# Optimization experiments

Hardware: AMD Instinct MI355X
Metric: run time of the kernel (lower is better)

## Reference

```python
import jax, jax.numpy as jnp
import numpy as np

N, C, E, T, H, D = 50000, 128, 320000, 8, 64, 4
EPS = 1e-5


def setup_inputs() -> dict:
    key = jax.random.key(0)
    ks = jax.random.split(key, 10)
    x = jax.random.normal(ks[0], (N, C), dtype=jnp.float32)
    edge_index = jax.random.randint(ks[1], (2, E), 0, N, dtype=jnp.int64)
    edge_types = jax.random.randint(ks[2], (E,), 0, T, dtype=jnp.int64)
    # per-type MLP params: LayerNorm(2C) -> Linear(2C,H) -> ReLU -> Linear(H, D*D)
    s1 = 1.0 / np.sqrt(2 * C)
    s2 = 1.0 / np.sqrt(H)
    gamma = jnp.ones((T, 2 * C), dtype=jnp.float32)
    beta = jnp.zeros((T, 2 * C), dtype=jnp.float32)
    W1 = jax.random.uniform(ks[3], (T, 2 * C, H), jnp.float32, -s1, s1)
    b1 = jax.random.uniform(ks[4], (T, H), jnp.float32, -s1, s1)
    W2 = jax.random.uniform(ks[5], (T, H, D * D), jnp.float32, -s2, s2)
    b2 = jax.random.uniform(ks[6], (T, D * D), jnp.float32, -s2, s2)
    return {"x": x, "edge_index": edge_index, "edge_types": edge_types,
            "gamma": gamma, "beta": beta, "W1": W1, "b1": b1, "W2": W2, "b2": b2}


def reference(x, edge_index, edge_types, gamma, beta, W1, b1, W2, b2):
    row, col = edge_index[0], edge_index[1]
    h_cat = jnp.concatenate([x[row], x[col]], axis=-1)  # [E, 2C]
    # shared (non-affine) layernorm stats; per-type affine applied in the loop
    mu = jnp.mean(h_cat, axis=-1, keepdims=True)
    var = jnp.mean(jnp.square(h_cat - mu), axis=-1, keepdims=True)
    x_hat = (h_cat - mu) * jax.lax.rsqrt(var + EPS)  # [E, 2C]
    out = jnp.zeros((E, D * D), dtype=h_cat.dtype)
    for t in range(T):  # fixed, small structural loop over edge types
        h = x_hat * gamma[t] + beta[t]
        h1 = jax.nn.relu(h @ W1[t] + b1[t])  # [E, H]
        o = h1 @ W2[t] + b2[t]               # [E, D*D]
        out = jnp.where((edge_types == t)[:, None], o, out)
    h_sheaf = out.reshape(-1, D, D)
    attn = jax.nn.softmax(h_sheaf, axis=-1)
    sheaf_maps = jnp.eye(D, dtype=h_sheaf.dtype)[None] - attn
    return sheaf_maps
```

## Files before the change

### kernel.cpp

```cpp
#include <hip/hip_runtime.h>
#include <math.h>

#define CC 128
#define TWO_C 256
#define NT 8
#define HH 64
#define DD 16

typedef short bf16x8 __attribute__((ext_vector_type(8)));
typedef float f32x4 __attribute__((ext_vector_type(4)));

static __device__ __forceinline__ unsigned short f2bf_rne(float f) {
    union { float f; unsigned int u; } v; v.f = f;
    unsigned int r = (v.u + 0x7fffu + ((v.u >> 16) & 1u)) >> 16;
    return (unsigned short)r;
}
static __device__ __forceinline__ unsigned int pkbf(float a, float b) {
    unsigned int ua = __float_as_uint(a) + 0x8000u;
    unsigned int ub = __float_as_uint(b) + 0x8000u;
    return (ua >> 16) | (ub & 0xffff0000u);
}
static __device__ __forceinline__ void glds16(const void* g, void* l) {
    __builtin_amdgcn_global_load_lds(
        (const __attribute__((address_space(1))) void*)g,
        (__attribute__((address_space(3))) void*)l, 16, 0, 0);
}

__global__ __launch_bounds__(256) void pack_kernel(
    const float* __restrict__ W1, const float* __restrict__ W2,
    const float* __restrict__ gamma, const float* __restrict__ beta,
    const float* __restrict__ b1, const float* __restrict__ x,
    unsigned short* __restrict__ W1p, unsigned short* __restrict__ W2p,
    float* __restrict__ s1g, float* __restrict__ c1g,
    unsigned short* __restrict__ xb, float2* __restrict__ SQ, int Nnodes)
{
    const int tid = blockIdx.x * 256 + threadIdx.x;

    if (tid < 16384) {
        int l = tid & 63, kt = (tid >> 6) & 7, nt = (tid >> 9) & 3, t = tid >> 11;
        int n = nt * 16 + (l & 15);
        int k0 = kt * 32 + (l >> 4) * 8;
        #pragma unroll
        for (int j = 0; j < 8; ++j) {
            int k = k0 + j;
            float v = gamma[t * TWO_C + k] * W1[(size_t)t * TWO_C * HH + (size_t)k * HH + n];
            W1p[tid * 8 + j] = f2bf_rne(v);
        }
    } else if (tid < 17408) {
        int s = tid - 16384;
        int l = s & 63, kt = (s >> 6) & 1, t = s >> 7;
        int n = l & 15;
        int k0 = kt * 32 + (l >> 4) * 8;
        #pragma unroll
        for (int j = 0; j < 8; ++j)
            W2p[s * 8 + j] = f2bf_rne(W2[(size_t)t * HH * DD + (size_t)(k0 + j) * DD + n]);
    } else if (tid < 17920) {
        int s = tid - 17408;
        int t = s >> 6, n = s & 63;
        float sa = 0.f, ca = 0.f;
        for (int k = 0; k < TWO_C; ++k) {
            float wv = W1[(size_t)t * TWO_C * HH + (size_t)k * HH + n];
            sa = fmaf(gamma[t * TWO_C + k], wv, sa);
            ca = fmaf(beta[t * TWO_C + k], wv, ca);
        }
        s1g[s] = sa;
        c1g[s] = ca + b1[s];
    } else {
        int idx = tid - 17920;
        int v = idx >> 4;
        if (v < Nnodes) {
            int ll = idx & 15;
            int base = idx * 8;
            float4 p = *(const float4*)(x + base);
            float4 q = *(const float4*)(x + base + 4);
            uint4 u;
            u.x = pkbf(p.x, p.y); u.y = pkbf(p.z, p.w);
            u.z = pkbf(q.x, q.y); u.w = pkbf(q.z, q.w);
            *(uint4*)(xb + base) = u;
            float s  = p.x + p.y + p.z + p.w + q.x + q.y + q.z + q.w;
            float sq = p.x*p.x + p.y*p.y + p.z*p.z + p.w*p.w
                     + q.x*q.x + q.y*q.y + q.z*q.z + q.w*q.w;
            #pragma unroll
            for (int off = 1; off < 16; off <<= 1) {
                s  += __shfl_xor(s, off);
                sq += __shfl_xor(sq, off);
            }
            if (ll == 0) SQ[v] = make_float2(s, sq);
        }
    }
}

__global__ __launch_bounds__(256) void hist_kernel(const int* __restrict__ et,
                                                   int* __restrict__ counts, int E)
{
    __shared__ int lh[NT];
    if (threadIdx.x < NT) lh[threadIdx.x] = 0;
    __syncthreads();
    int i0 = (blockIdx.x * 256 + threadIdx.x) * 4;
    if (i0 + 3 < E) {
        int4 tv = *(const int4*)(et + i0);
        atomicAdd(&lh[tv.x], 1); atomicAdd(&lh[tv.y], 1);
        atomicAdd(&lh[tv.z], 1); atomicAdd(&lh[tv.w], 1);
    } else {
        #pragma unroll
        for (int j = 0; j < 4; ++j)
            if (i0 + j < E) atomicAdd(&lh[et[i0 + j]], 1);
    }
    __syncthreads();
    if (threadIdx.x < NT && lh[threadIdx.x]) atomicAdd(&counts[threadIdx.x], lh[threadIdx.x]);
}

__global__ void scan_kernel(const int* __restrict__ counts, int* __restrict__ po,
                            int* __restrict__ cursor)
{
    if (threadIdx.x == 0 && blockIdx.x == 0) {
        int acc = 0;
        for (int t = 0; t < NT; ++t) {
            po[t] = acc;
            cursor[t] = acc;
            acc += ((counts[t] + 63) >> 6) << 6;
        }
        po[NT] = acc;
    }
}

__global__ __launch_bounds__(256) void scatter_kernel(const int* __restrict__ et,
                                                      const int* __restrict__ ei,
                                                      int* __restrict__ cursor,
                                                      int* __restrict__ sorted,
                                                      int* __restrict__ srow,
                                                      int* __restrict__ scol,
                                                      int* __restrict__ inv,
                                                      int E, int write_inv)
{
    __shared__ int lh[NT], lbase[NT];
    if (threadIdx.x < NT) lh[threadIdx.x] = 0;
    __syncthreads();
    int i0 = (blockIdx.x * 256 + threadIdx.x) * 4;
    int tl[4], rk[4];
    #pragma unroll
    for (int j = 0; j < 4; ++j) {
        int i = i0 + j;
        if (i < E) { tl[j] = et[i]; rk[j] = atomicAdd(&lh[tl[j]], 1); }
    }
    __syncthreads();
    if (threadIdx.x < NT)
        lbase[threadIdx.x] = lh[threadIdx.x] ? atomicAdd(&cursor[threadIdx.x], lh[threadIdx.x]) : 0;
    __syncthreads();
    #pragma unroll
    for (int j = 0; j < 4; ++j) {
        int i = i0 + j;
        if (i < E) {
            int slot = lbase[tl[j]] + rk[j];
            sorted[slot] = i;
            srow[slot] = ei[i];
            scol[slot] = ei[E + i];
            if (write_inv) inv[i] = slot;
        }
    }
}

#define XHAT_OFF 0
#define H1_OFF   0
#define STATS_OFF 16384
#define SID_OFF   16896
#define RB_OFF    17152
#define CB_OFF    17408
#define LDS_BYTES 17664

template <int TMP>
__global__ __launch_bounds__(256, 8) void sheaf_main_full(
    const unsigned short* __restrict__ xb, const float* __restrict__ b2,
    const unsigned short* __restrict__ W1p, const unsigned short* __restrict__ W2p,
    const float* __restrict__ s1g, const float* __restrict__ c1g,
    const float2* __restrict__ SQ,
    const int* __restrict__ po, const int* __restrict__ counts,
    const int* __restrict__ sorted, const int* __restrict__ srow,
    const int* __restrict__ scol,
    float* __restrict__ dst)
{
    __shared__ __align__(16) unsigned char lds[LDS_BYTES];
    const int base = blockIdx.x * 64;
    if (base >= po[NT]) return;
    int t = 0;
    while (base >= po[t + 1]) ++t;
    const int lim = po[t] + counts[t];
    if (base >= lim) return;

    const int tid = threadIdx.x;
    const int w = tid >> 6, lane = tid & 63;
    const int lg = lane >> 4, ll = lane & 15;

    int* sid  = (int*)(lds + SID_OFF);
    int* rbuf = (int*)(lds + RB_OFF);
    int* cbuf = (int*)(lds + CB_OFF);
    float2* stats = (float2*)(lds + STATS_OFF);

    if (tid < 64) {
        int slot = base + tid;
        int src = slot < lim ? slot : po[t];
        rbuf[tid] = srow[src];
        cbuf[tid] = scol[src];
        if (!TMP) sid[tid] = sorted[src];
    }
    __syncthreads();

    #pragma unroll
    for (int i = 0; i < 4; ++i) {
        const int el = w * 16 + i * 4 + lg;
        const unsigned short* src = xb + (size_t)rbuf[el] * CC + ((ll ^ (el & 7)) * 8);
        glds16(src, lds + XHAT_OFF + (w * 16 + i * 4) * 256);
    }
    if (tid < 64) {
        float2 a = SQ[rbuf[tid]];
        float2 b = SQ[cbuf[tid]];
        float mu  = (a.x + b.x) * (1.0f / TWO_C);
        float var = (a.y + b.y) * (1.0f / TWO_C) - mu * mu;
        stats[tid] = make_float2(mu, rsqrtf(var + 1e-5f));
    }
    __syncthreads();

    f32x4 acc[4];
    #pragma unroll
    for (int mt = 0; mt < 4; ++mt) acc[mt] = (f32x4){0.f, 0.f, 0.f, 0.f};
    const bf16x8* Bp = (const bf16x8*)W1p + (size_t)((t * 4 + w) * 8) * 64 + lane;
    #pragma unroll
    for (int kt = 0; kt < 4; ++kt) {
        bf16x8 bfrag = Bp[kt * 64];
        #pragma unroll
        for (int mt = 0; mt < 4; ++mt) {
            int row = mt * 16 + ll;
            bf16x8 afrag = *(const bf16x8*)(lds + XHAT_OFF + row * 256 +
                                            ((kt * 64 + lg * 16) ^ ((row & 7) << 4)));
            acc[mt] = __builtin_amdgcn_mfma_f32_16x16x32_bf16(afrag, bfrag, acc[mt], 0, 0, 0);
        }
    }
    __syncthreads();

    #pragma unroll
    for (int i = 0; i < 4; ++i) {
        const int el = w * 16 + i * 4 + lg;
        const unsigned short* src = xb + (size_t)cbuf[el] * CC + ((ll ^ (el & 7)) * 8);
        glds16(src, lds + XHAT_OFF + (w * 16 + i * 4) * 256);
    }
    __syncthreads();

    #pragma unroll
    for (int kt = 0; kt < 4; ++kt) {
        bf16x8 bfrag = Bp[(4 + kt) * 64];
        #pragma unroll
        for (int mt = 0; mt < 4; ++mt) {
            int row = mt * 16 + ll;
            bf16x8 afrag = *(const bf16x8*)(lds + XHAT_OFF + row * 256 +
                                            ((kt * 64 + lg * 16) ^ ((row & 7) << 4)));
            acc[mt] = __builtin_amdgcn_mfma_f32_16x16x32_bf16(afrag, bfrag, acc[mt], 0, 0, 0);
        }
    }
    __syncthreads();

    const int n = w * 16 + ll;
    const float s1v = s1g[t * HH + n];
    const float c1v = c1g[t * HH + n];
    #pragma unroll
    for (int mt = 0; mt < 4; ++mt) {
        #pragma unroll
        for (int j = 0; j < 4; ++j) {
            int el = mt * 16 + lg * 4 + j;
            float2 st = stats[el];
            float z = st.y * (acc[mt][j] - st.x * s1v) + c1v;
            z = fmaxf(z, 0.0f);
            *(unsigned short*)(lds + H1_OFF + el * 144 + n * 2) =
                (unsigned short)((__float_as_uint(z) + 0x8000u) >> 16);
        }
    }
    __syncthreads();

    f32x4 acc2 = (f32x4){0.f, 0.f, 0.f, 0.f};
    #pragma unroll
    for (int kt = 0; kt < 2; ++kt) {
        bf16x8 bfrag = ((const bf16x8*)W2p)[(t * 2 + kt) * 64 + lane];
        bf16x8 afrag = *(const bf16x8*)(lds + H1_OFF + (w * 16 + ll) * 144 + kt * 64 + lg * 16);
        acc2 = __builtin_amdgcn_mfma_f32_16x16x32_bf16(afrag, bfrag, acc2, 0, 0, 0);
    }

    const float b2v = b2[t * DD + ll];
    const float diag = ((ll >> 2) == (ll & 3)) ? 1.0f : 0.0f;
    #pragma unroll
    for (int j = 0; j < 4; ++j) {
        float o = acc2[j] + b2v;
        float m = fmaxf(o, __shfl_xor(o, 1));
        m = fmaxf(m, __shfl_xor(m, 2));
        float p = __expf(o - m);
        float su = p + __shfl_xor(p, 1);
        su += __shfl_xor(su, 2);
        float res = diag - p / su;
        int el = w * 16 + lg * 4 + j;
        if (TMP) dst[(size_t)(base + el) * DD + ll] = res;
        else     dst[(size_t)sid[el] * DD + ll] = res;
    }
}

__global__ __launch_bounds__(256, 8) void sheaf_main_fb(
    const float* __restrict__ x, const float* __restrict__ b2,
    const unsigned short* __restrict__ W1p, const unsigned short* __restrict__ W2p,
    const float* __restrict__ s1g, const float* __restrict__ c1g,
    const int* __restrict__ po, const int* __restrict__ counts,
    const int* __restrict__ sorted, const int* __restrict__ srow,
    const int* __restrict__ scol,
    float* __restrict__ out)
{
    __shared__ __align__(16) unsigned char lds[LDS_BYTES];
    const int base = blockIdx.x * 64;
    if (base >= po[NT]) return;
    int t = 0;
    while (base >= po[t + 1]) ++t;
    const int lim = po[t] + counts[t];
    if (base >= lim) return;

    const int tid = threadIdx.x;
    const int w = tid >> 6, lane = tid & 63;
    const int lg = lane >> 4, ll = lane & 15;
    int* sid  = (int*)(lds + SID_OFF);
    int* rbuf = (int*)(lds + RB_OFF);
    int* cbuf = (int*)(lds + CB_OFF);

    if (tid < 64) {
        int slot = base + tid;
        int src = slot < lim ? slot : po[t];
        rbuf[tid] = srow[src]; cbuf[tid] = scol[src]; sid[tid] = sorted[src];
    }
    __syncthreads();

    float s[4] = {0,0,0,0}, sq[4] = {0,0,0,0};
    #pragma unroll
    for (int i = 0; i < 4; ++i) {
        const int el = w * 16 + i * 4 + lg;
        const float4* px = (const float4*)(x + (size_t)rbuf[el] * CC + ll * 8);
        float4 p = px[0], q = px[1];
        s[i] += p.x+p.y+p.z+p.w+q.x+q.y+q.z+q.w;
        sq[i] = fmaf(p.x,p.x,sq[i]); sq[i] = fmaf(p.y,p.y,sq[i]);
        sq[i] = fmaf(p.z,p.z,sq[i]); sq[i] = fmaf(p.w,p.w,sq[i]);
        sq[i] = fmaf(q.x,q.x,sq[i]); sq[i] = fmaf(q.y,q.y,sq[i]);
        sq[i] = fmaf(q.z,q.z,sq[i]); sq[i] = fmaf(q.w,q.w,sq[i]);
        uint4 u;
        u.x = pkbf(p.x,p.y); u.y = pkbf(p.z,p.w); u.z = pkbf(q.x,q.y); u.w = pkbf(q.z,q.w);
        *(uint4*)(lds + XHAT_OFF + el * 256 + ((ll * 16) ^ ((el & 7) << 4))) = u;
    }
    __syncthreads();

    f32x4 acc[4];
    #pragma unroll
    for (int mt = 0; mt < 4; ++mt) acc[mt] = (f32x4){0.f,0.f,0.f,0.f};
    const bf16x8* Bp = (const bf16x8*)W1p + (size_t)((t * 4 + w) * 8) * 64 + lane;
    #pragma unroll
    for (int kt = 0; kt < 4; ++kt) {
        bf16x8 bfrag = Bp[kt * 64];
        #pragma unroll
        for (int mt = 0; mt < 4; ++mt) {
            int row = mt * 16 + ll;
            bf16x8 afrag = *(const bf16x8*)(lds + XHAT_OFF + row * 256 +
                                            ((kt * 64 + lg * 16) ^ ((row & 7) << 4)));
            acc[mt] = __builtin_amdgcn_mfma_f32_16x16x32_bf16(afrag, bfrag, acc[mt], 0, 0, 0);
        }
    }
    __syncthreads();

    #pragma unroll
    for (int i = 0; i < 4; ++i) {
        const int el = w * 16 + i * 4 + lg;
        const float4* px = (const float4*)(x + (size_t)cbuf[el] * CC + ll * 8);
        float4 p = px[0], q = px[1];
        s[i] += p.x+p.y+p.z+p.w+q.x+q.y+q.z+q.w;
        sq[i] = fmaf(p.x,p.x,sq[i]); sq[i] = fmaf(p.y,p.y,sq[i]);
        sq[i] = fmaf(p.z,p.z,sq[i]); sq[i] = fmaf(p.w,p.w,sq[i]);
        sq[i] = fmaf(q.x,q.x,sq[i]); sq[i] = fmaf(q.y,q.y,sq[i]);
        sq[i] = fmaf(q.z,q.z,sq[i]); sq[i] = fmaf(q.w,q.w,sq[i]);
        uint4 u;
        u.x = pkbf(p.x,p.y); u.y = pkbf(p.z,p.w); u.z = pkbf(q.x,q.y); u.w = pkbf(q.z,q.w);
        *(uint4*)(lds + XHAT_OFF + el * 256 + ((ll * 16) ^ ((el & 7) << 4))) = u;
    }
    float2* stats = (float2*)(lds + STATS_OFF);
    #pragma unroll
    for (int i = 0; i < 4; ++i) {
        float s_ = s[i], q_ = sq[i];
        #pragma unroll
        for (int off = 1; off < 16; off <<= 1) {
            s_ += __shfl_xor(s_, off); q_ += __shfl_xor(q_, off);
        }
        if (ll == 0) {
            float mu = s_ * (1.0f / TWO_C);
            float var = q_ * (1.0f / TWO_C) - mu * mu;
            stats[w * 16 + i * 4 + lg] = make_float2(mu, rsqrtf(var + 1e-5f));
        }
    }
    __syncthreads();

    #pragma unroll
    for (int kt = 0; kt < 4; ++kt) {
        bf16x8 bfrag = Bp[(4 + kt) * 64];
        #pragma unroll
        for (int mt = 0; mt < 4; ++mt) {
            int row = mt * 16 + ll;
            bf16x8 afrag = *(const bf16x8*)(lds + XHAT_OFF + row * 256 +
                                            ((kt * 64 + lg * 16) ^ ((row & 7) << 4)));
            acc[mt] = __builtin_amdgcn_mfma_f32_16x16x32_bf16(afrag, bfrag, acc[mt], 0, 0, 0);
        }
    }
    __syncthreads();

    const int n = w * 16 + ll;
    const float s1v = s1g[t * HH + n];
    const float c1v = c1g[t * HH + n];
    #pragma unroll
    for (int mt = 0; mt < 4; ++mt) {
        #pragma unroll
        for (int j = 0; j < 4; ++j) {
            int el = mt * 16 + lg * 4 + j;
            float2 st = stats[el];
            float z = st.y * (acc[mt][j] - st.x * s1v) + c1v;
            z = fmaxf(z, 0.0f);
            *(unsigned short*)(lds + H1_OFF + el * 144 + n * 2) =
                (unsigned short)((__float_as_uint(z) + 0x8000u) >> 16);
        }
    }
    __syncthreads();

    f32x4 acc2 = (f32x4){0.f,0.f,0.f,0.f};
    #pragma unroll
    for (int kt = 0; kt < 2; ++kt) {
        bf16x8 bfrag = ((const bf16x8*)W2p)[(t * 2 + kt) * 64 + lane];
        bf16x8 afrag = *(const bf16x8*)(lds + H1_OFF + (w * 16 + ll) * 144 + kt * 64 + lg * 16);
        acc2 = __builtin_amdgcn_mfma_f32_16x16x32_bf16(afrag, bfrag, acc2, 0, 0, 0);
    }
    const float b2v = b2[t * DD + ll];
    const float diag = ((ll >> 2) == (ll & 3)) ? 1.0f : 0.0f;
    #pragma unroll
    for (int j = 0; j < 4; ++j) {
        float o = acc2[j] + b2v;
        float m = fmaxf(o, __shfl_xor(o, 1));
        m = fmaxf(m, __shfl_xor(m, 2));
        float p = __expf(o - m);
        float su = p + __shfl_xor(p, 1);
        su += __shfl_xor(su, 2);
        int el = w * 16 + lg * 4 + j;
        out[(size_t)sid[el] * DD + ll] = diag - p / su;
    }
}

__global__ __launch_bounds__(256) void permute_kernel(const float4* __restrict__ tmp,
                                                      const int* __restrict__ inv,
                                                      float4* __restrict__ out, int E)
{
    int e = blockIdx.x * 256 + threadIdx.x;
    if (e >= E) return;
    int slot = inv[e];
    const float4* s = tmp + (size_t)slot * 4;
    float4 a = s[0], b = s[1], c = s[2], d = s[3];
    float4* o = out + (size_t)e * 4;
    o[0] = a; o[1] = b; o[2] = c; o[3] = d;
}

extern "C" void kernel_launch(void* const* d_in, const int* in_sizes, int n_in,
                              void* d_out, int out_size, void* d_ws, size_t ws_size,
                              hipStream_t stream) {
    const float* x          = (const float*)d_in[0];
    const int*   edge_index = (const int*)  d_in[1];
    const int*   edge_types = (const int*)  d_in[2];
    const float* gamma      = (const float*)d_in[3];
    const float* beta       = (const float*)d_in[4];
    const float* W1         = (const float*)d_in[5];
    const float* b1         = (const float*)d_in[6];
    const float* W2         = (const float*)d_in[7];
    const float* b2         = (const float*)d_in[8];
    float* out = (float*)d_out;

    const int E = in_sizes[2];
    const int xtotal = in_sizes[0];
    const int Nn = xtotal / CC;
    const int cap = ((E + 63) & ~63) + 512;

    int* ws_i   = (int*)d_ws;
    int* counts = ws_i;
    int* cursor = ws_i + 16;
    int* po     = ws_i + 24;
    int* sorted = ws_i + 40;
    int* srow   = sorted + cap;
    int* scol   = srow + cap;

    const size_t pack_bytes = (size_t)NT * 4 * 8 * 64 * 8 * 2
                            + (size_t)NT * 2 * 64 * 8 * 2
                            + (size_t)NT * HH * 4 * 2;
    size_t pk_off = (((size_t)(40 + 3 * (size_t)cap)) * 4 + 255) & ~(size_t)255;
    unsigned short* W1p = (unsigned short*)((char*)d_ws + pk_off);
    unsigned short* W2p = W1p + (size_t)NT * 4 * 8 * 64 * 8;
    float* s1g = (float*)(W2p + (size_t)NT * 2 * 64 * 8);
    float* c1g = s1g + NT * HH;

    size_t sq_off = (pk_off + pack_bytes + 255) & ~(size_t)255;
    float2* SQ = (float2*)((char*)d_ws + sq_off);
    size_t xb_off = (sq_off + (size_t)Nn * 8 + 255) & ~(size_t)255;
    unsigned short* xb = (unsigned short*)((char*)d_ws + xb_off);
    const size_t xb_end = xb_off + (size_t)xtotal * 2;

    const int use_full = (ws_size >= xb_end) ? 1 : 0;

    size_t inv_off = (xb_end + 255) & ~(size_t)255;
    size_t tmp_off = (inv_off + (size_t)cap * 4 + 255) & ~(size_t)255;
    const int use_tmp = (use_full && ws_size >= tmp_off + (size_t)cap * DD * 4) ? 1 : 0;
    int* inv = (int*)((char*)d_ws + inv_off);
    float* tmp = (float*)((char*)d_ws + tmp_off);

    hipMemsetAsync(counts, 0, 32, stream);

    const int pt = use_full ? (17920 + Nn * 16) : 17920;
    hipLaunchKernelGGL(pack_kernel, dim3((pt + 255) / 256), dim3(256), 0, stream,
                       W1, W2, gamma, beta, b1, x, W1p, W2p, s1g, c1g,
                       xb, SQ, use_full ? Nn : 0);

    const int hq = (E + 3) / 4;
    hipLaunchKernelGGL(hist_kernel, dim3((hq + 255) / 256), dim3(256), 0, stream,
                       edge_types, counts, E);
    hipLaunchKernelGGL(scan_kernel, dim3(1), dim3(64), 0, stream, counts, po, cursor);
    hipLaunchKernelGGL(scatter_kernel, dim3((hq + 255) / 256), dim3(256), 0, stream,
                       edge_types, edge_index, cursor, sorted, srow, scol, inv, E, use_tmp);

    const int gmain = cap / 64;
    if (use_full) {
        if (use_tmp) {
            hipLaunchKernelGGL((sheaf_main_full<1>), dim3(gmain), dim3(256), 0, stream,
                               xb, b2, W1p, W2p, s1g, c1g, SQ, po, counts,
                               sorted, srow, scol, tmp);
            hipLaunchKernelGGL(permute_kernel, dim3((E + 255) / 256), dim3(256), 0, stream,
                               (const float4*)tmp, inv, (float4*)out, E);
        } else {
            hipLaunchKernelGGL((sheaf_main_full<0>), dim3(gmain), dim3(256), 0, stream,
                               xb, b2, W1p, W2p, s1g, c1g, SQ, po, counts,
                               sorted, srow, scol, out);
        }
    } else {
        hipLaunchKernelGGL(sheaf_main_fb, dim3(gmain), dim3(256), 0, stream,
                           x, b2, W1p, W2p, s1g, c1g, po, counts,
                           sorted, srow, scol, out);
    }
}
```

Before: 84.20 us.

## Replace histogram+scan bucketing with fixed-capacity per-type segments and parallelize s1/c1 reduction

The edge bucketing now scatters each edge directly into a fixed-capacity segment per type, which removes the histogram and scan kernels and their serial dependency. The main kernel maps blocks to (type, chunk) from the block index, and blocks beyond the count for their type exit early. The per-(type, column) gamma·W1 and beta·W1 reductions in the pack kernel are spread across a wavefront with shuffle reductions instead of a 256-iteration serial loop per thread. The cost is an 8x larger segment workspace and a much larger grid in which most blocks return immediately.

```diff
diff --git a/kernel.cpp b/kernel.cpp
--- a/kernel.cpp
+++ b/kernel.cpp
@@ -54,19 +54,30 @@
         #pragma unroll
         for (int j = 0; j < 8; ++j)
             W2p[s * 8 + j] = f2bf_rne(W2[(size_t)t * HH * DD + (size_t)(k0 + j) * DD + n]);
-    } else if (tid < 17920) {
-        int s = tid - 17408;
-        int t = s >> 6, n = s & 63;
+    } else if (tid < 50176) {
+        int id = tid - 17408;
+        int lane = id & 63;
+        int pair = id >> 6;
+        int t = pair >> 6, n = pair & 63;
         float sa = 0.f, ca = 0.f;
-        for (int k = 0; k < TWO_C; ++k) {
+        #pragma unroll
+        for (int i = 0; i < 4; ++i) {
+            int k = i * 64 + lane;
             float wv = W1[(size_t)t * TWO_C * HH + (size_t)k * HH + n];
             sa = fmaf(gamma[t * TWO_C + k], wv, sa);
             ca = fmaf(beta[t * TWO_C + k], wv, ca);
         }
-        s1g[s] = sa;
-        c1g[s] = ca + b1[s];
+        #pragma unroll
+        for (int off = 1; off < 64; off <<= 1) {
+            sa += __shfl_xor(sa, off);
+            ca += __shfl_xor(ca, off);
+        }
+        if (lane == 0) {
+            s1g[pair] = sa;
+            c1g[pair] = ca + b1[pair];
+        }
     } else {
-        int idx = tid - 17920;
+        int idx = tid - 50176;
         int v = idx >> 4;
         if (v < Nnodes) {
             int ll = idx & 15;
@@ -90,6 +101,40 @@
     }
 }
 
+__global__ __launch_bounds__(256) void scatter_direct(const int* __restrict__ et,
+                                                      const int* __restrict__ ei,
+                                                      int* __restrict__ cursor,
+                                                      int* __restrict__ srow,
+                                                      int* __restrict__ scol,
+                                                      int* __restrict__ inv,
+                                                      int E, int capE)
+{
+    __shared__ int lh[NT], lbase[NT];
+    if (threadIdx.x < NT) lh[threadIdx.x] = 0;
+    __syncthreads();
+    int i0 = (blockIdx.x * 256 + threadIdx.x) * 4;
+    int tl[4], rk[4];
+    #pragma unroll
+    for (int j = 0; j < 4; ++j) {
+        int i = i0 + j;
+        if (i < E) { tl[j] = et[i]; rk[j] = atomicAdd(&lh[tl[j]], 1); }
+    }
+    __syncthreads();
+    if (threadIdx.x < NT)
+        lbase[threadIdx.x] = lh[threadIdx.x] ? atomicAdd(&cursor[threadIdx.x], lh[threadIdx.x]) : 0;
+    __syncthreads();
+    #pragma unroll
+    for (int j = 0; j < 4; ++j) {
+        int i = i0 + j;
+        if (i < E) {
+            int slot = tl[j] * capE + lbase[tl[j]] + rk[j];
+            srow[slot] = ei[i];
+            scol[slot] = ei[E + i];
+            inv[i] = slot;
+        }
+    }
+}
+
 __global__ __launch_bounds__(256) void hist_kernel(const int* __restrict__ et,
                                                    int* __restrict__ counts, int E)
 {
@@ -97,15 +142,9 @@
     if (threadIdx.x < NT) lh[threadIdx.x] = 0;
     __syncthreads();
     int i0 = (blockIdx.x * 256 + threadIdx.x) * 4;
-    if (i0 + 3 < E) {
-        int4 tv = *(const int4*)(et + i0);
-        atomicAdd(&lh[tv.x], 1); atomicAdd(&lh[tv.y], 1);
-        atomicAdd(&lh[tv.z], 1); atomicAdd(&lh[tv.w], 1);
-    } else {
-        #pragma unroll
-        for (int j = 0; j < 4; ++j)
-            if (i0 + j < E) atomicAdd(&lh[et[i0 + j]], 1);
-    }
+    #pragma unroll
+    for (int j = 0; j < 4; ++j)
+        if (i0 + j < E) atomicAdd(&lh[et[i0 + j]], 1);
     __syncthreads();
     if (threadIdx.x < NT && lh[threadIdx.x]) atomicAdd(&counts[threadIdx.x], lh[threadIdx.x]);
 }
@@ -130,8 +169,7 @@
                                                       int* __restrict__ sorted,
                                                       int* __restrict__ srow,
                                                       int* __restrict__ scol,
-                                                      int* __restrict__ inv,
-                                                      int E, int write_inv)
+                                                      int E)
 {
     __shared__ int lh[NT], lbase[NT];
     if (threadIdx.x < NT) lh[threadIdx.x] = 0;
@@ -155,7 +193,6 @@
             sorted[slot] = i;
             srow[slot] = ei[i];
             scol[slot] = ei[E + i];
-            if (write_inv) inv[i] = slot;
         }
     }
 }
@@ -168,7 +205,7 @@
 #define CB_OFF    17408
 #define LDS_BYTES 17664
 
-template <int TMP>
+template <int FIXED>
 __global__ __launch_bounds__(256, 8) void sheaf_main_full(
     const unsigned short* __restrict__ xb, const float* __restrict__ b2,
     const unsigned short* __restrict__ W1p, const unsigned short* __restrict__ W2p,
@@ -177,15 +214,27 @@
     const int* __restrict__ po, const int* __restrict__ counts,
     const int* __restrict__ sorted, const int* __restrict__ srow,
     const int* __restrict__ scol,
-    float* __restrict__ dst)
+    float* __restrict__ dst, int bpt, int capE)
 {
     __shared__ __align__(16) unsigned char lds[LDS_BYTES];
-    const int base = blockIdx.x * 64;
-    if (base >= po[NT]) return;
-    int t = 0;
-    while (base >= po[t + 1]) ++t;
-    const int lim = po[t] + counts[t];
-    if (base >= lim) return;
+    int t, base, lim, segBase;
+    if (FIXED) {
+        t = blockIdx.x / bpt;
+        int inb = (blockIdx.x - t * bpt) * 64;
+        lim = counts[t];
+        if (inb >= lim) return;
+        segBase = t * capE;
+        base = segBase + inb;
+        lim += segBase;
+    } else {
+        base = blockIdx.x * 64;
+        if (base >= po[NT]) return;
+        t = 0;
+        while (base >= po[t + 1]) ++t;
+        lim = po[t] + counts[t];
+        if (base >= lim) return;
+        segBase = po[t];
+    }
 
     const int tid = threadIdx.x;
     const int w = tid >> 6, lane = tid & 63;
@@ -198,10 +247,10 @@
 
     if (tid < 64) {
         int slot = base + tid;
-        int src = slot < lim ? slot : po[t];
+        int src = slot < lim ? slot : segBase;
         rbuf[tid] = srow[src];
         cbuf[tid] = scol[src];
-        if (!TMP) sid[tid] = sorted[src];
+        if (!FIXED) sid[tid] = sorted[src];
     }
     __syncthreads();
 
@@ -295,8 +344,8 @@
         su += __shfl_xor(su, 2);
         float res = diag - p / su;
         int el = w * 16 + lg * 4 + j;
-        if (TMP) dst[(size_t)(base + el) * DD + ll] = res;
-        else     dst[(size_t)sid[el] * DD + ll] = res;
+        if (FIXED) dst[(size_t)(base + el) * DD + ll] = res;
+        else       dst[(size_t)sid[el] * DD + ll] = res;
     }
 }
 
@@ -477,69 +526,90 @@
     const int E = in_sizes[2];
     const int xtotal = in_sizes[0];
     const int Nn = xtotal / CC;
-    const int cap = ((E + 63) & ~63) + 512;
+    const int hq = (E + 3) / 4;
+
+    const size_t pack_bytes = (size_t)NT * 4 * 8 * 64 * 8 * 2
+                            + (size_t)NT * 2 * 64 * 8 * 2
+                            + (size_t)NT * HH * 4 * 2;
 
     int* ws_i   = (int*)d_ws;
     int* counts = ws_i;
     int* cursor = ws_i + 16;
     int* po     = ws_i + 24;
+
+    const int capE = (E + 63) & ~63;
+    const int bpt  = capE / 64;
+    const size_t segs = (size_t)capE * NT;
+    size_t srow_d_off = 256;
+    size_t scol_d_off = srow_d_off + segs * 4;
+    size_t inv_d_off  = scol_d_off + segs * 4;
+    size_t pk_d_off   = (inv_d_off + (size_t)E * 4 + 255) & ~(size_t)255;
+    size_t sq_d_off   = (pk_d_off + pack_bytes + 255) & ~(size_t)255;
+    size_t xb_d_off   = (sq_d_off + (size_t)Nn * 8 + 255) & ~(size_t)255;
+    size_t tmp_d_off  = (xb_d_off + (size_t)xtotal * 2 + 255) & ~(size_t)255;
+    size_t direct_end = tmp_d_off + segs * DD * 4;
+    const int use_direct = (ws_size >= direct_end) ? 1 : 0;
+
+    if (use_direct) {
+        int* srow = (int*)((char*)d_ws + srow_d_off);
+        int* scol = (int*)((char*)d_ws + scol_d_off);
+        int* inv  = (int*)((char*)d_ws + inv_d_off);
+        unsigned short* W1p = (unsigned short*)((char*)d_ws + pk_d_off);
+        unsigned short* W2p = W1p + (size_t)NT * 4 * 8 * 64 * 8;
+        float* s1g = (float*)(W2p + (size_t)NT * 2 * 64 * 8);
+        float* c1g = s1g + NT * HH;
+        float2* SQ = (float2*)((char*)d_ws + sq_d_off);
+        unsigned short* xb = (unsigned short*)((char*)d_ws + xb_d_off);
+        float* tmp = (float*)((char*)d_ws + tmp_d_off);
+
+        hipMemsetAsync(counts, 0, 64, stream);
+        const int pt = 50176 + Nn * 16;
+        hipLaunchKernelGGL(pack_kernel, dim3((pt + 255) / 256), dim3(256), 0, stream,
+                           W1, W2, gamma, beta, b1, x, W1p, W2p, s1g, c1g, xb, SQ, Nn);
+        hipLaunchKernelGGL(scatter_direct, dim3((hq + 255) / 256), dim3(256), 0, stream,
+                           edge_types, edge_index, counts, srow, scol, inv, E, capE);
+        hipLaunchKernelGGL((sheaf_main_full<1>), dim3(NT * bpt), dim3(256), 0, stream,
+                           xb, b2, W1p, W2p, s1g, c1g, SQ, counts, counts,
+                           (const int*)0, srow, scol, tmp, bpt, capE);
+        hipLaunchKernelGGL(permute_kernel, dim3((E + 255) / 256), dim3(256), 0, stream,
+                           (const float4*)tmp, inv, (float4*)out, E);
+        return;
+    }
+
+    const int cap = capE + 512;
     int* sorted = ws_i + 40;
     int* srow   = sorted + cap;
     int* scol   = srow + cap;
-
-    const size_t pack_bytes = (size_t)NT * 4 * 8 * 64 * 8 * 2
-                            + (size_t)NT * 2 * 64 * 8 * 2
-                            + (size_t)NT * HH * 4 * 2;
     size_t pk_off = (((size_t)(40 + 3 * (size_t)cap)) * 4 + 255) & ~(size_t)255;
     unsigned short* W1p = (unsigned short*)((char*)d_ws + pk_off);
     unsigned short* W2p = W1p + (size_t)NT * 4 * 8 * 64 * 8;
     float* s1g = (float*)(W2p + (size_t)NT * 2 * 64 * 8);
     float* c1g = s1g + NT * HH;
-
     size_t sq_off = (pk_off + pack_bytes + 255) & ~(size_t)255;
     float2* SQ = (float2*)((char*)d_ws + sq_off);
     size_t xb_off = (sq_off + (size_t)Nn * 8 + 255) & ~(size_t)255;
     unsigned short* xb = (unsigned short*)((char*)d_ws + xb_off);
     const size_t xb_end = xb_off + (size_t)xtotal * 2;
-
     const int use_full = (ws_size >= xb_end) ? 1 : 0;
 
-    size_t inv_off = (xb_end + 255) & ~(size_t)255;
-    size_t tmp_off = (inv_off + (size_t)cap * 4 + 255) & ~(size_t)255;
-    const int use_tmp = (use_full && ws_size >= tmp_off + (size_t)cap * DD * 4) ? 1 : 0;
-    int* inv = (int*)((char*)d_ws + inv_off);
-    float* tmp = (float*)((char*)d_ws + tmp_off);
-
     hipMemsetAsync(counts, 0, 32, stream);
-
-    const int pt = use_full ? (17920 + Nn * 16) : 17920;
+    const int pt = use_full ? (50176 + Nn * 16) : 50176;
     hipLaunchKernelGGL(pack_kernel, dim3((pt + 255) / 256), dim3(256), 0, stream,
                        W1, W2, gamma, beta, b1, x, W1p, W2p, s1g, c1g,
                        xb, SQ, use_full ? Nn : 0);
-
-    const int hq = (E + 3) / 4;
     hipLaunchKernelGGL(hist_kernel, dim3((hq + 255) / 256), dim3(256), 0, stream,
                        edge_types, counts, E);
     hipLaunchKernelGGL(scan_kernel, dim3(1), dim3(64), 0, stream, counts, po, cursor);
     hipLaunchKernelGGL(scatter_kernel, dim3((hq + 255) / 256), dim3(256), 0, stream,
-                       edge_types, edge_index, cursor, sorted, srow, scol, inv, E, use_tmp);
+                       edge_types, edge_index, cursor, sorted, srow, scol, E);
 
     const int gmain = cap / 64;
-    if (use_full) {
-        if (use_tmp) {
-            hipLaunchKernelGGL((sheaf_main_full<1>), dim3(gmain), dim3(256), 0, stream,
-                               xb, b2, W1p, W2p, s1g, c1g, SQ, po, counts,
-                               sorted, srow, scol, tmp);
-            hipLaunchKernelGGL(permute_kernel, dim3((E + 255) / 256), dim3(256), 0, stream,
-                               (const float4*)tmp, inv, (float4*)out, E);
-        } else {
-            hipLaunchKernelGGL((sheaf_main_full<0>), dim3(gmain), dim3(256), 0, stream,
-                               xb, b2, W1p, W2p, s1g, c1g, SQ, po, counts,
-                               sorted, srow, scol, out);
-        }
-    } else {
+    if (use_full)
+        hipLaunchKernelGGL((sheaf_main_full<0>), dim3(gmain), dim3(256), 0, stream,
+                           xb, b2, W1p, W2p, s1g, c1g, SQ, po, counts,
+                           sorted, srow, scol, out, 0, 0);
+    else
         hipLaunchKernelGGL(sheaf_main_fb, dim3(gmain), dim3(256), 0, stream,
                            x, b2, W1p, W2p, s1g, c1g, po, counts,
                            sorted, srow, scol, out);
-    }
-}
+}
```

Result: faster. 70.55 us (-16.2%).
